# Optimization experiments

Hardware: AMD Instinct MI355X
Metric: run time of the kernel (lower is better)

Reference implementation:

```python
import jax, jax.numpy as jnp
import numpy as np
import math

# real<->complex packing matching the module's _c2r/_r2c (trailing dim 2)
def _r2c(x):
    return x[..., 0] + 1j * x[..., 1]

H, N, CH, RANK, LMAX = 256, 64, 1, 1, 2048


def setup_inputs() -> dict:
    key = jax.random.key(0)
    k0, k1, k2, k3, k4, k5 = jax.random.split(key, 6)
    C = jax.random.normal(k0, (CH, H, N, 2), jnp.float32)
    B = jax.random.normal(k1, (1, H, N, 2), jnp.float32)
    P = 0.3 * jax.random.normal(k2, (RANK, H, N, 2), jnp.float32)
    # w must have negative real part (Hurwitz) so Cauchy denominators stay away from zero
    w_re = -(jnp.abs(jax.random.normal(k3, (H, N))) * 0.5 + 0.1)
    w_im = jnp.pi * jax.random.normal(k4, (H, N))
    w = jnp.stack([w_re, w_im], axis=-1).astype(jnp.float32)
    log_dt = jax.random.uniform(k5, (H,), jnp.float32,
                                math.log(1e-3), math.log(1e-1))
    return {"C": C, "B": B, "P": P, "w": w, "log_dt": log_dt, "L": LMAX}


def reference(C, B, P, w, log_dt, L):
    Cc = _r2c(C)            # (c, H, N) complex
    Bc = _r2c(B)            # (1, H, N)
    Pc = _r2c(P)            # (r, H, N)
    wc = _r2c(w)            # (H, N)
    Qc = jnp.conj(Pc)       # Q = P.conj() (resolve_conj path)
    dt = jnp.exp(log_dt)    # (H,)

    # FFT nodes + bilinear transform (rate == 1.0)
    F = L // 2 + 1
    omega = jnp.exp(-2j * jnp.pi / L) ** jnp.arange(F)   # (F,) complex64
    z = 2 * (1 - omega) / (1 + omega)                     # (F,)

    w_dt = wc * dt[:, None].astype(wc.dtype)              # (H, N)

    Bcat = jnp.concatenate([Bc, Pc], axis=0)              # (1+r, H, N)
    Ccat = jnp.concatenate([Cc, Qc], axis=0)              # (c+r, H, N)
    v = Bcat[:, None] * Ccat[None]                        # (1+r, c+r, H, N)

    # Cauchy kernel: r[a,b,h,f] = sum_n v[a,b,h,n] / (z[f] - w_dt[h,n])
    denom = z - w_dt[..., None]                           # (H, N, F)
    r = jnp.sum(v[..., None] / denom, axis=-2)            # (1+r, c+r, H, F)
    r = r * dt[None, None, :, None].astype(r.dtype)

    # rank-1 Woodbury low-rank correction
    k_f = r[:-1, :-1] - r[:-1, -1:] * r[-1:, :-1] / (1 + r[-1:, -1:])  # (1, c, H, F)
    k_f = k_f * 2 / (1 + omega)

    k = jnp.fft.irfft(k_f, n=L, axis=-1)[..., :L]         # (1, c, H, L) real
    k_B = k[-1]                                           # (c, H, L)
    return k_B
```

## Files before the change

kernel.cpp:

```cpp
#include <hip/hip_runtime.h>


typedef float v2f __attribute__((ext_vector_type(2)));

#define HH 256
#define NN 64
#define LL 2048
#define MM 1024
#define NT 512

#define PI_OVER_1024 0.0030679615757712823f
#define PI_OVER_512  0.0061359231515425647f

__global__ __launch_bounds__(NT) void ssk_fused(
    const float* __restrict__ Cin, const float* __restrict__ Bin,
    const float* __restrict__ Pin, const float* __restrict__ Win,
    const float* __restrict__ logdt, float* __restrict__ out)
{
    __shared__ float4 sD4[NN * 3];
    __shared__ float2 sX[MM + 1];
    __shared__ float2 sA[MM];
    __shared__ float2 sBf[MM];

    const int h = blockIdx.x;
    const int t = threadIdx.x;
    const float dtv = __expf(logdt[h]);

    if (t < NN) {
        const int base = (h * NN + t) * 2;
        const float Br = Bin[base], Bi = Bin[base + 1];
        const float Cr = Cin[base], Ci = Cin[base + 1];
        const float Pr = Pin[base], Pi = Pin[base + 1];
        const float v00r = Br * Cr - Bi * Ci, v00i = Br * Ci + Bi * Cr;
        sD4[t * 3 + 0] = make_float4(Win[base] * dtv, Win[base + 1] * dtv, v00r, v00i);
        sD4[t * 3 + 1] = make_float4(Br * Pr + Bi * Pi, Bi * Pr - Br * Pi,
                                     Pr * Cr - Pi * Ci, Pr * Ci + Pi * Cr);
        sD4[t * 3 + 2] = make_float4(Pr * Pr + Pi * Pi, 0.f, 0.f, 0.f);
        float r = v00r;
        #pragma unroll
        for (int off = 32; off; off >>= 1) r += __shfl_xor(r, off, 64);
        if (t == 0) sX[MM] = make_float2(0.5f * dtv * r, 0.f);
    }
    __syncthreads();

    const float* sDf = (const float*)sD4;
    #pragma unroll
    for (int rep = 0; rep < 2; ++rep) {
        const int f = t + rep * 512;
        float si, co;
        __sincosf(PI_OVER_1024 * (float)f, &si, &co);
        const v2f u  = {1.0f + co, -si};
        const v2f t1 = {2.0f * (1.0f - co), 2.0f * si};

        v2f s00 = {0.f, 0.f}, s01 = {0.f, 0.f}, s10 = {0.f, 0.f}, s11 = {0.f, 0.f};
        #pragma unroll 8
        for (int n = 0; n < NN; ++n) {
            const float4 q0 = sD4[n * 3 + 0];
            const float4 q1 = sD4[n * 3 + 1];
            const float v11 = sDf[n * 12 + 8];
            v2f den = t1;
            den = den - (v2f){q0.x, q0.x} * u;
            den = den + (v2f){q0.y, q0.y} * (v2f){u.y, -u.x};
            const float inv = __builtin_amdgcn_rcpf(den.x * den.x + den.y * den.y);
            const v2f e  = den * (v2f){inv, -inv};
            const v2f es = {e.y, e.x};
            s00 = s00 + (v2f){q0.z, q0.z} * e;
            s00 = s00 + (v2f){-q0.w, q0.w} * es;
            s01 = s01 + (v2f){q1.x, q1.x} * e;
            s01 = s01 + (v2f){-q1.y, q1.y} * es;
            s10 = s10 + (v2f){q1.z, q1.z} * e;
            s10 = s10 + (v2f){-q1.w, q1.w} * es;
            s11 = s11 + (v2f){v11, v11} * e;
        }
        const float gr = dtv * u.x, gi = dtv * u.y;
        const float numr = s01.x * s10.x - s01.y * s10.y;
        const float numi = s01.x * s10.y + s01.y * s10.x;
        const float qr = 1.0f + (gr * s11.x - gi * s11.y);
        const float qi = gr * s11.y + gi * s11.x;
        const float tr = gr * numr - gi * numi;
        const float ti = gr * numi + gi * numr;
        const float qinv = __builtin_amdgcn_rcpf(qr * qr + qi * qi);
        const float cr = (tr * qr + ti * qi) * qinv;
        const float ci = (ti * qr - tr * qi) * qinv;
        const float kr = 2.0f * dtv * (s00.x - cr);
        float       ki = 2.0f * dtv * (s00.y - ci);
        if (f == 0) ki = 0.0f;
        sX[f] = make_float2(kr, ki);
    }
    __syncthreads();

    const float HS = 4.8828125e-4f;
    for (int f = t; f < MM; f += NT) {
        const float2 a1 = sX[f];
        const float2 x2 = sX[MM - f];
        const float er  = HS * (a1.x + x2.x), eim = HS * (a1.y - x2.y);
        const float gr  = HS * (a1.x - x2.x), gim = HS * (a1.y + x2.y);
        float st, ct;
        __sincosf(PI_OVER_1024 * (float)f, &st, &ct);
        const float Or = ct * gr - st * gim;
        const float Oi = ct * gim + st * gr;
        sA[f] = make_float2(er - Oi, eim + Or);
    }
    __syncthreads();

    float2* cur = sA;
    float2* nxt = sBf;
    #pragma unroll
    for (int i = 0; i < 10; ++i) {
        const int s = 1 << i;
        const int b = t;
        const int j = b & ~(s - 1);
        const float2 a = cur[b];
        const float2 c = cur[b + 512];
        const float sr = a.x + c.x, sim = a.y + c.y;
        const float dr = a.x - c.x, dim = a.y - c.y;
        float st, ct;
        __sincosf(PI_OVER_512 * (float)j, &st, &ct);
        nxt[b + j]     = make_float2(sr, sim);
        nxt[b + j + s] = make_float2(ct * dr - st * dim, ct * dim + st * dr);
        __syncthreads();
        float2* tmp = cur; cur = nxt; nxt = tmp;
    }

    float2* outv = (float2*)(out + (size_t)h * LL);
    for (int m = t; m < MM; m += NT) outv[m] = cur[m];
}

extern "C" void kernel_launch(void* const* d_in, const int* in_sizes, int n_in,
                              void* d_out, int out_size, void* d_ws, size_t ws_size,
                              hipStream_t stream) {
    const float* C  = (const float*)d_in[0];
    const float* B  = (const float*)d_in[1];
    const float* P  = (const float*)d_in[2];
    const float* W  = (const float*)d_in[3];
    const float* ld = (const float*)d_in[4];
    float* out = (float*)d_out;
    ssk_fused<<<HH, NT, 0, stream>>>(C, B, P, W, ld, out);
}
```

Baseline: 77.03 us.

## Halve block threads and compute four frequencies per thread in Cauchy loop

Reduces the block from 512 to 256 threads, and each thread now evaluates four frequency points at once in the Cauchy summation. Each LDS load of the per-node coefficients is therefore reused across four frequencies, which cuts shared-memory traffic and load instructions per frequency. The FFT stages and output loop are adapted so each thread handles two butterflies per stage. In exchange, per-thread register use and ILP rise, and fewer resident threads per block may reduce latency hiding in the barrier-heavy FFT part.

```diff
diff --git a/kernel.cpp b/kernel.cpp
--- a/kernel.cpp
+++ b/kernel.cpp
@@ -7,7 +7,8 @@
 #define NN 64
 #define LL 2048
 #define MM 1024
-#define NT 512
+#define NT 256
+#define FPT 4
 
 #define PI_OVER_1024 0.0030679615757712823f
 #define PI_OVER_512  0.0061359231515425647f
@@ -43,54 +44,67 @@
     }
     __syncthreads();
 
-    const float* sDf = (const float*)sD4;
-    #pragma unroll
-    for (int rep = 0; rep < 2; ++rep) {
-        const int f = t + rep * 512;
-        float si, co;
-        __sincosf(PI_OVER_1024 * (float)f, &si, &co);
-        const v2f u  = {1.0f + co, -si};
-        const v2f t1 = {2.0f * (1.0f - co), 2.0f * si};
-
-        v2f s00 = {0.f, 0.f}, s01 = {0.f, 0.f}, s10 = {0.f, 0.f}, s11 = {0.f, 0.f};
-        #pragma unroll 8
+    {
+        const float* sDf = (const float*)sD4;
+        v2f u[FPT], t1[FPT];
+        v2f s00[FPT], s01[FPT], s10[FPT], s11[FPT];
+        #pragma unroll
+        for (int rep = 0; rep < FPT; ++rep) {
+            const int f = t + rep * NT;
+            float si, co;
+            __sincosf(PI_OVER_1024 * (float)f, &si, &co);
+            u[rep]  = (v2f){1.0f + co, -si};
+            t1[rep] = (v2f){2.0f * (1.0f - co), 2.0f * si};
+            s00[rep] = (v2f){0.f, 0.f}; s01[rep] = (v2f){0.f, 0.f};
+            s10[rep] = (v2f){0.f, 0.f}; s11[rep] = (v2f){0.f, 0.f};
+        }
+        #pragma unroll 4
         for (int n = 0; n < NN; ++n) {
             const float4 q0 = sD4[n * 3 + 0];
             const float4 q1 = sD4[n * 3 + 1];
             const float v11 = sDf[n * 12 + 8];
-            v2f den = t1;
-            den = den - (v2f){q0.x, q0.x} * u;
-            den = den + (v2f){q0.y, q0.y} * (v2f){u.y, -u.x};
-            const float inv = __builtin_amdgcn_rcpf(den.x * den.x + den.y * den.y);
-            const v2f e  = den * (v2f){inv, -inv};
-            const v2f es = {e.y, e.x};
-            s00 = s00 + (v2f){q0.z, q0.z} * e;
-            s00 = s00 + (v2f){-q0.w, q0.w} * es;
-            s01 = s01 + (v2f){q1.x, q1.x} * e;
-            s01 = s01 + (v2f){-q1.y, q1.y} * es;
-            s10 = s10 + (v2f){q1.z, q1.z} * e;
-            s10 = s10 + (v2f){-q1.w, q1.w} * es;
-            s11 = s11 + (v2f){v11, v11} * e;
+            #pragma unroll
+            for (int rep = 0; rep < FPT; ++rep) {
+                v2f den = t1[rep];
+                den = den - (v2f){q0.x, q0.x} * u[rep];
+                den = den + (v2f){q0.y, q0.y} * (v2f){u[rep].y, -u[rep].x};
+                const float inv = __builtin_amdgcn_rcpf(den.x * den.x + den.y * den.y);
+                const v2f e  = den * (v2f){inv, -inv};
+                const v2f es = {e.y, e.x};
+                s00[rep] = s00[rep] + (v2f){q0.z, q0.z} * e;
+                s00[rep] = s00[rep] + (v2f){-q0.w, q0.w} * es;
+                s01[rep] = s01[rep] + (v2f){q1.x, q1.x} * e;
+                s01[rep] = s01[rep] + (v2f){-q1.y, q1.y} * es;
+                s10[rep] = s10[rep] + (v2f){q1.z, q1.z} * e;
+                s10[rep] = s10[rep] + (v2f){-q1.w, q1.w} * es;
+                s11[rep] = s11[rep] + (v2f){v11, v11} * e;
+            }
         }
-        const float gr = dtv * u.x, gi = dtv * u.y;
-        const float numr = s01.x * s10.x - s01.y * s10.y;
-        const float numi = s01.x * s10.y + s01.y * s10.x;
-        const float qr = 1.0f + (gr * s11.x - gi * s11.y);
-        const float qi = gr * s11.y + gi * s11.x;
-        const float tr = gr * numr - gi * numi;
-        const float ti = gr * numi + gi * numr;
-        const float qinv = __builtin_amdgcn_rcpf(qr * qr + qi * qi);
-        const float cr = (tr * qr + ti * qi) * qinv;
-        const float ci = (ti * qr - tr * qi) * qinv;
-        const float kr = 2.0f * dtv * (s00.x - cr);
-        float       ki = 2.0f * dtv * (s00.y - ci);
-        if (f == 0) ki = 0.0f;
-        sX[f] = make_float2(kr, ki);
+        #pragma unroll
+        for (int rep = 0; rep < FPT; ++rep) {
+            const int f = t + rep * NT;
+            const float gr = dtv * u[rep].x, gi = dtv * u[rep].y;
+            const float numr = s01[rep].x * s10[rep].x - s01[rep].y * s10[rep].y;
+            const float numi = s01[rep].x * s10[rep].y + s01[rep].y * s10[rep].x;
+            const float qr = 1.0f + (gr * s11[rep].x - gi * s11[rep].y);
+            const float qi = gr * s11[rep].y + gi * s11[rep].x;
+            const float tr = gr * numr - gi * numi;
+            const float ti = gr * numi + gi * numr;
+            const float qinv = __builtin_amdgcn_rcpf(qr * qr + qi * qi);
+            const float cr = (tr * qr + ti * qi) * qinv;
+            const float ci = (ti * qr - tr * qi) * qinv;
+            const float kr = 2.0f * dtv * (s00[rep].x - cr);
+            float       ki = 2.0f * dtv * (s00[rep].y - ci);
+            if (f == 0) ki = 0.0f;
+            sX[f] = make_float2(kr, ki);
+        }
     }
     __syncthreads();
 
     const float HS = 4.8828125e-4f;
-    for (int f = t; f < MM; f += NT) {
+    #pragma unroll
+    for (int rep = 0; rep < FPT; ++rep) {
+        const int f = t + rep * NT;
         const float2 a1 = sX[f];
         const float2 x2 = sX[MM - f];
         const float er  = HS * (a1.x + x2.x), eim = HS * (a1.y - x2.y);
@@ -108,22 +122,29 @@
     #pragma unroll
     for (int i = 0; i < 10; ++i) {
         const int s = 1 << i;
-        const int b = t;
-        const int j = b & ~(s - 1);
-        const float2 a = cur[b];
-        const float2 c = cur[b + 512];
-        const float sr = a.x + c.x, sim = a.y + c.y;
-        const float dr = a.x - c.x, dim = a.y - c.y;
-        float st, ct;
-        __sincosf(PI_OVER_512 * (float)j, &st, &ct);
-        nxt[b + j]     = make_float2(sr, sim);
-        nxt[b + j + s] = make_float2(ct * dr - st * dim, ct * dim + st * dr);
+        #pragma unroll
+        for (int half = 0; half < 2; ++half) {
+            const int b = t + half * NT;
+            const int j = b & ~(s - 1);
+            const float2 a = cur[b];
+            const float2 c = cur[b + 512];
+            const float sr = a.x + c.x, sim = a.y + c.y;
+            const float dr = a.x - c.x, dim = a.y - c.y;
+            float st, ct;
+            __sincosf(PI_OVER_512 * (float)j, &st, &ct);
+            nxt[b + j]     = make_float2(sr, sim);
+            nxt[b + j + s] = make_float2(ct * dr - st * dim, ct * dim + st * dr);
+        }
         __syncthreads();
         float2* tmp = cur; cur = nxt; nxt = tmp;
     }
 
     float2* outv = (float2*)(out + (size_t)h * LL);
-    for (int m = t; m < MM; m += NT) outv[m] = cur[m];
+    #pragma unroll
+    for (int rep = 0; rep < FPT; ++rep) {
+        const int m = t + rep * NT;
+        outv[m] = cur[m];
+    }
 }
 
 extern "C" void kernel_launch(void* const* d_in, const int* in_sizes, int n_in,
```

Result: faster. 75.24 us (-2.3%).
